# Optimization experiments

Hardware: AMD Instinct MI355X
Metric: run time of the kernel (lower is better)

The kernel has to match this reference:

```python
import jax, jax.numpy as jnp
import numpy as np

B, T, D = 4, 2048, 1024

def setup_inputs() -> dict:
    key = jax.random.key(0)
    kx, kq, kk, kv = jax.random.split(key, 4)
    return {
        "vector": jax.random.normal(kx, (B, T, D), dtype=jnp.float32),
        # original uses torch.rand -> uniform [0,1)
        "W_queries": jax.random.uniform(kq, (D, D), dtype=jnp.float32),
        "W_keys": jax.random.uniform(kk, (D, D), dtype=jnp.float32),
        "W_values": jax.random.uniform(kv, (D, D), dtype=jnp.float32),
    }

def reference(vector, W_queries, W_keys, W_values):
    b, num_token, d_out = vector.shape
    queries = vector @ W_queries          # [b, t, d]
    keys = vector @ W_keys                # [b, t, d]
    values = vector @ W_values            # [b, t, d]
    # attention_score: [b, q, k]
    scores = jnp.einsum('bqd,bkd->bqk', queries, keys)
    causal_mask = jnp.triu(jnp.ones((num_token, num_token), dtype=bool), k=1)
    scores = jnp.where(causal_mask[None, :, :], -jnp.inf, scores)
    # NOTE: original uses FLOOR division `//` by sqrt(d_k) -- faithful here.
    inv_sqrt_scale = jnp.asarray(np.sqrt(keys.shape[-1]), dtype=scores.dtype)
    weights = jnp.floor(scores / inv_sqrt_scale)
    # NOTE: original applies softmax over dim=1 (the query axis), not dim=-1.
    weights = jax.nn.softmax(weights, axis=1)
    # dropout rate is 0.0 (eval/deterministic): identity
    context = jnp.einsum('bqk,bkd->bqd', weights, values)
    return context
```

## Files before the change

### kernel.cpp

```cpp
#include <hip/hip_runtime.h>
#include <math.h>

typedef _Float16 half4 __attribute__((ext_vector_type(4)));
typedef _Float16 half8 __attribute__((ext_vector_type(8)));
typedef float f32x4 __attribute__((ext_vector_type(4)));

#define GLD16(gptr, lptr)                                                     \
    __builtin_amdgcn_global_load_lds(                                         \
        (const __attribute__((address_space(1))) unsigned int*)(gptr),        \
        (__attribute__((address_space(3))) unsigned int*)(lptr), 16, 0, 0)

#define WAIT_VM(N) asm volatile("s_waitcnt vmcnt(" #N ")" ::: "memory")
#define BARRIER()  __builtin_amdgcn_s_barrier()
#define SCHED_FENCE() __builtin_amdgcn_sched_barrier(0)

namespace {

constexpr int Bb = 4;
constexpr int Tt = 2048;
constexpr int Dd = 1024;
constexpr int BT = Bb * Tt;
constexpr int NCH = 16;

__device__ inline _Float16 f2h(float f) { return (_Float16)f; }

__global__ __launch_bounds__(256) void convert_all_kernel(
    const float* __restrict__ X,  const float* __restrict__ Wq,
    const float* __restrict__ Wk, const float* __restrict__ Wv,
    _Float16* __restrict__ Xhi, _Float16* __restrict__ Xlo,
    _Float16* __restrict__ Wqh, _Float16* __restrict__ Wql,
    _Float16* __restrict__ Wkh, _Float16* __restrict__ Wkl,
    _Float16* __restrict__ WvTh)
{
    __shared__ float tile[64][65];
    const int f = blockIdx.x;
    if (f < 8192) {
        const int idx = f * 1024 + threadIdx.x * 4;
        const float4 v = *(const float4*)(X + idx);
        const float a[4] = {v.x, v.y, v.z, v.w};
        half4 h, l;
#pragma unroll
        for (int i = 0; i < 4; ++i) {
            h[i] = f2h(a[i]);
            l[i] = f2h(a[i] - (float)h[i]);
        }
        *(half4*)(Xhi + idx) = h;
        *(half4*)(Xlo + idx) = l;
    } else if (f < 10240) {
        const int g = f - 8192;
        const int mat = g >> 10;
        const float* W = mat ? Wk : Wq;
        _Float16* Hh = mat ? Wkh : Wqh;
        _Float16* Ll = mat ? Wkl : Wql;
        const int idx = (g & 1023) * 1024 + threadIdx.x * 4;
        const float4 v = *(const float4*)(W + idx);
        const float a[4] = {v.x, v.y, v.z, v.w};
        half4 h, l;
#pragma unroll
        for (int i = 0; i < 4; ++i) {
            h[i] = f2h(a[i]);
            l[i] = f2h(a[i] - (float)h[i]);
        }
        *(half4*)(Hh + idx) = h;
        *(half4*)(Ll + idx) = l;
    } else {
        const int g = f - 10240;
        const int n0 = (g & 15) * 64, k0 = (g >> 4) * 64;
        const int tx = threadIdx.x & 63, ty = threadIdx.x >> 6;
#pragma unroll
        for (int i = 0; i < 16; ++i)
            tile[ty + i * 4][tx] = Wv[(size_t)(k0 + ty + i * 4) * Dd + n0 + tx];
        __syncthreads();
#pragma unroll
        for (int i = 0; i < 16; ++i) {
            const float v = tile[tx][ty + i * 4];
            WvTh[(size_t)(n0 + ty + i * 4) * Dd + k0 + tx] = f2h(v);
        }
    }
}

__global__ __launch_bounds__(256) void gt_kernel(
    const _Float16* __restrict__ Wkh, const _Float16* __restrict__ Wkl,
    const _Float16* __restrict__ Wqh, const _Float16* __restrict__ Wql,
    _Float16* __restrict__ GTh, _Float16* __restrict__ GTl)
{
    __shared__ _Float16 Ahl[2][2][4][512];
    __shared__ _Float16 Bhl[2][2][4][512];

    const int n0 = blockIdx.x * 64;
    const int m0 = blockIdx.y * 64;
    const int tid = threadIdx.x;
    const int w = tid >> 6, lane = tid & 63;
    const int lr = lane & 15, lq = lane >> 4;
    const int wi = (w >> 1) * 2, wj = (w & 1) * 2;

    f32x4 acc[2][2];
#pragma unroll
    for (int i = 0; i < 2; ++i)
#pragma unroll
        for (int j = 0; j < 2; ++j)
#pragma unroll
            for (int c = 0; c < 4; ++c) acc[i][j][c] = 0.f;

    auto stage = [&](int bf, int kk) {
        const int s = w;
        const size_t ar = (size_t)(m0 + s * 16 + lr) * Dd + kk + lq * 8;
        const size_t br = (size_t)(n0 + s * 16 + lr) * Dd + kk + lq * 8;
        GLD16(Wkh + ar, &Ahl[bf][0][s][0]);
        GLD16(Wkl + ar, &Ahl[bf][1][s][0]);
        GLD16(Wqh + br, &Bhl[bf][0][s][0]);
        GLD16(Wql + br, &Bhl[bf][1][s][0]);
    };

    stage(0, 0);
    int ib = 0;
    for (int step = 0; step < 32; ++step, ib ^= 1) {
        if (step < 31) {
            stage(ib ^ 1, (step + 1) << 5);
            WAIT_VM(4);
        } else {
            WAIT_VM(0);
        }
        BARRIER();
        SCHED_FENCE();
        half8 ah[2], al[2], bh[2], bl[2];
#pragma unroll
        for (int i = 0; i < 2; ++i) {
            ah[i] = *(const half8*)&Ahl[ib][0][wi + i][lane * 8];
            al[i] = *(const half8*)&Ahl[ib][1][wi + i][lane * 8];
        }
#pragma unroll
        for (int j = 0; j < 2; ++j) {
            bh[j] = *(const half8*)&Bhl[ib][0][wj + j][lane * 8];
            bl[j] = *(const half8*)&Bhl[ib][1][wj + j][lane * 8];
        }
#pragma unroll
        for (int i = 0; i < 2; ++i)
#pragma unroll
            for (int j = 0; j < 2; ++j) {
                acc[i][j] = __builtin_amdgcn_mfma_f32_16x16x32_f16(ah[i], bh[j], acc[i][j], 0, 0, 0);
                acc[i][j] = __builtin_amdgcn_mfma_f32_16x16x32_f16(ah[i], bl[j], acc[i][j], 0, 0, 0);
                acc[i][j] = __builtin_amdgcn_mfma_f32_16x16x32_f16(al[i], bh[j], acc[i][j], 0, 0, 0);
            }
        BARRIER();
    }

#pragma unroll
    for (int i = 0; i < 2; ++i)
#pragma unroll
        for (int r = 0; r < 4; ++r) {
            const int row = m0 + (wi + i) * 16 + lq * 4 + r;
#pragma unroll
            for (int j = 0; j < 2; ++j) {
                const int col = n0 + (wj + j) * 16 + lr;
                const float v = acc[i][j][r];
                const _Float16 h = f2h(v);
                GTh[(size_t)row * Dd + col] = h;
                GTl[(size_t)row * Dd + col] = f2h(v - (float)h);
            }
        }
}

__global__ __launch_bounds__(256, 2) void tv_kernel(
    const _Float16* __restrict__ Xhi, const _Float16* __restrict__ Xlo,
    const _Float16* __restrict__ GTh, const _Float16* __restrict__ GTl,
    const _Float16* __restrict__ WvTh,
    _Float16* __restrict__ Thi, _Float16* __restrict__ Tlo,
    _Float16* __restrict__ Vt)
{
    __shared__ _Float16 smem[32768];
    auto A_ = [&](int bf, int hl, int s) -> _Float16* {
        return smem + ((bf * 2 + hl) * 8 + s) * 512;
    };
    auto B_ = [&](int bf, int hl, int s) -> _Float16* {
        return smem + 16384 + ((bf * 2 + hl) * 8 + s) * 512;
    };

    const int f  = blockIdx.x;
    const int fp = (f & 7) * 128 + (f >> 3);
    const int mb  = fp >> 4;
    const int sub = fp & 15;
    const int m0 = mb * 128;
    const int n0 = (sub & 7) * 128;

    const int tid = threadIdx.x;
    const int w = tid >> 6, lane = tid & 63;
    const int lr = lane & 15, lq = lane >> 4;
    const int wr = (w >> 1) * 4, wc = (w & 1) * 4;

    f32x4 acc[4][4];
#pragma unroll
    for (int i = 0; i < 4; ++i)
#pragma unroll
        for (int j = 0; j < 4; ++j)
#pragma unroll
            for (int c = 0; c < 4; ++c) acc[i][j][c] = 0.f;

    if (sub < 8) {
        auto stage = [&](int bf, int kk) {
#pragma unroll
            for (int s2 = 0; s2 < 2; ++s2) {
                const int s = w * 2 + s2;
                const size_t ar = (size_t)(m0 + s * 16 + lr) * Dd + kk + lq * 8;
                const size_t br = (size_t)(n0 + s * 16 + lr) * Dd + kk + lq * 8;
                GLD16(Xhi + ar, A_(bf, 0, s));
                GLD16(Xlo + ar, A_(bf, 1, s));
                GLD16(GTh + br, B_(bf, 0, s));
                GLD16(GTl + br, B_(bf, 1, s));
            }
        };
        stage(0, 0);
        int ib = 0;
        for (int step = 0; step < 32; ++step, ib ^= 1) {
            if (step < 31) {
                stage(ib ^ 1, (step + 1) << 5);
                WAIT_VM(8);
            } else {
                WAIT_VM(0);
            }
            BARRIER();
            SCHED_FENCE();
            half8 ah[4], al[4], bh[4], bl[4];
#pragma unroll
            for (int i = 0; i < 4; ++i) {
                ah[i] = *(const half8*)(A_(ib, 0, wr + i) + lane * 8);
                al[i] = *(const half8*)(A_(ib, 1, wr + i) + lane * 8);
            }
#pragma unroll
            for (int j = 0; j < 4; ++j) {
                bh[j] = *(const half8*)(B_(ib, 0, wc + j) + lane * 8);
                bl[j] = *(const half8*)(B_(ib, 1, wc + j) + lane * 8);
            }
#pragma unroll
            for (int i = 0; i < 4; ++i)
#pragma unroll
                for (int j = 0; j < 4; ++j) {
                    acc[i][j] = __builtin_amdgcn_mfma_f32_16x16x32_f16(ah[i], bh[j], acc[i][j], 0, 0, 0);
                    acc[i][j] = __builtin_amdgcn_mfma_f32_16x16x32_f16(ah[i], bl[j], acc[i][j], 0, 0, 0);
                    acc[i][j] = __builtin_amdgcn_mfma_f32_16x16x32_f16(al[i], bh[j], acc[i][j], 0, 0, 0);
                }
            BARRIER();
        }
#pragma unroll
        for (int i = 0; i < 4; ++i)
#pragma unroll
            for (int r = 0; r < 4; ++r) {
                const int row = m0 + (wr + i) * 16 + lq * 4 + r;
#pragma unroll
                for (int j = 0; j < 4; ++j) {
                    const int col = n0 + (wc + j) * 16 + lr;
                    const float v = acc[i][j][r];
                    const _Float16 h = f2h(v);
                    Thi[(size_t)row * Dd + col] = h;
                    Tlo[(size_t)row * Dd + col] = f2h(v - (float)h);
                }
            }
    } else {
        auto stage = [&](int bf, int kk) {
#pragma unroll
            for (int s2 = 0; s2 < 2; ++s2) {
                const int s = w * 2 + s2;
                GLD16(Xhi + (size_t)(m0 + s * 16 + lr) * Dd + kk + lq * 8, A_(bf, 0, s));
                GLD16(WvTh + (size_t)(n0 + s * 16 + lr) * Dd + kk + lq * 8, B_(bf, 0, s));
            }
        };
        stage(0, 0);
        int ib = 0;
        for (int step = 0; step < 32; ++step, ib ^= 1) {
            if (step < 31) {
                stage(ib ^ 1, (step + 1) << 5);
                WAIT_VM(4);
            } else {
                WAIT_VM(0);
            }
            BARRIER();
            SCHED_FENCE();
            half8 a[4], b2[4];
#pragma unroll
            for (int i = 0; i < 4; ++i) a[i] = *(const half8*)(A_(ib, 0, wr + i) + lane * 8);
#pragma unroll
            for (int j = 0; j < 4; ++j) b2[j] = *(const half8*)(B_(ib, 0, wc + j) + lane * 8);
#pragma unroll
            for (int i = 0; i < 4; ++i)
#pragma unroll
                for (int j = 0; j < 4; ++j)
                    acc[i][j] = __builtin_amdgcn_mfma_f32_16x16x32_f16(a[i], b2[j], acc[i][j], 0, 0, 0);
            BARRIER();
        }
        __syncthreads();
#pragma unroll
        for (int i = 0; i < 4; ++i)
#pragma unroll
            for (int r2 = 0; r2 < 4; ++r2) {
                const int rloc = (wr + i) * 16 + lq * 4 + r2;
#pragma unroll
                for (int j = 0; j < 4; ++j) {
                    const int cloc = (wc + j) * 16 + lr;
                    smem[cloc * 136 + rloc] = f2h(acc[i][j][r2]);
                }
            }
        __syncthreads();
        const int b2i = m0 >> 11;
        const int t0  = m0 & 2047;
        const int dloc = tid >> 1, tl = (tid & 1) * 64;
        _Float16* vp = Vt + (size_t)b2i * Dd * Tt + (size_t)(n0 + dloc) * Tt + t0 + tl;
#pragma unroll
        for (int e = 0; e < 8; ++e)
            *(half8*)(vp + e * 8) = *(const half8*)&smem[dloc * 136 + tl + e * 8];
    }
}

__global__ __launch_bounds__(256, 2) void scores_mfma_kernel(
    const _Float16* __restrict__ Thi, const _Float16* __restrict__ Tlo,
    const _Float16* __restrict__ Xhi, const _Float16* __restrict__ Xlo,
    _Float16* __restrict__ Pp, float* __restrict__ Pm, float* __restrict__ Pl)
{
    const int f  = blockIdx.x;
    const int fp = (f & 7) * 68 + (f >> 3);
    const int b = fp / 136;
    const int t = fp - b * 136;
    int byi = (int)((sqrtf(8.f * t + 1.f) - 1.f) * 0.5f);
    if ((byi + 1) * (byi + 2) / 2 <= t) ++byi;
    if (byi * (byi + 1) / 2 > t) --byi;
    const int bxi = t - byi * (byi + 1) / 2;
    const int j0 = bxi * 128, q0 = byi * 128;
    _Float16* Pb = Pp + (size_t)b * Tt * Tt;

    __shared__ _Float16 Ahl[2][2][8][512];
    __shared__ _Float16 Bhl[2][2][8][512];
    const _Float16* Th = Thi + (size_t)b * Tt * Dd;
    const _Float16* Tl = Tlo + (size_t)b * Tt * Dd;
    const _Float16* Xh = Xhi + (size_t)b * Tt * Dd;
    const _Float16* Xl = Xlo + (size_t)b * Tt * Dd;

    const int tid = threadIdx.x;
    const int w = tid >> 6, lane = tid & 63;
    const int lr = lane & 15, lq = lane >> 4;
    const int wr = (w >> 1) * 4, wc = (w & 1) * 4;

    f32x4 acc[4][4];
#pragma unroll
    for (int i = 0; i < 4; ++i)
#pragma unroll
        for (int j = 0; j < 4; ++j)
#pragma unroll
            for (int c = 0; c < 4; ++c) acc[i][j][c] = 0.f;

    auto stage = [&](int bf, int kk) {
#pragma unroll
        for (int s2 = 0; s2 < 2; ++s2) {
            const int s = w * 2 + s2;
            const size_t ar = (size_t)(q0 + s * 16 + lr) * Dd + kk + lq * 8;
            const size_t br = (size_t)(j0 + s * 16 + lr) * Dd + kk + lq * 8;
            GLD16(Th + ar, &Ahl[bf][0][s][0]);
            GLD16(Tl + ar, &Ahl[bf][1][s][0]);
            GLD16(Xh + br, &Bhl[bf][0][s][0]);
            GLD16(Xl + br, &Bhl[bf][1][s][0]);
        }
    };

    stage(0, 0);
    int ib = 0;
    for (int step = 0; step < 32; ++step, ib ^= 1) {
        if (step < 31) {
            stage(ib ^ 1, (step + 1) << 5);
            WAIT_VM(8);
        } else {
            WAIT_VM(0);
        }
        BARRIER();
        SCHED_FENCE();
        half8 ah[4], al[4], bh[4], bl[4];
#pragma unroll
        for (int i = 0; i < 4; ++i) {
            ah[i] = *(const half8*)&Ahl[ib][0][wr + i][lane * 8];
            al[i] = *(const half8*)&Ahl[ib][1][wr + i][lane * 8];
        }
#pragma unroll
        for (int j = 0; j < 4; ++j) {
            bh[j] = *(const half8*)&Bhl[ib][0][wc + j][lane * 8];
            bl[j] = *(const half8*)&Bhl[ib][1][wc + j][lane * 8];
        }
#pragma unroll
        for (int i = 0; i < 4; ++i)
#pragma unroll
            for (int j = 0; j < 4; ++j) {
                acc[i][j] = __builtin_amdgcn_mfma_f32_16x16x32_f16(ah[i], bh[j], acc[i][j], 0, 0, 0);
                acc[i][j] = __builtin_amdgcn_mfma_f32_16x16x32_f16(ah[i], bl[j], acc[i][j], 0, 0, 0);
                acc[i][j] = __builtin_amdgcn_mfma_f32_16x16x32_f16(al[i], bh[j], acc[i][j], 0, 0, 0);
            }
        BARRIER();
    }

    float sv[4][4][4];
#pragma unroll
    for (int i = 0; i < 4; ++i)
#pragma unroll
        for (int r = 0; r < 4; ++r) {
            const int q = q0 + (wr + i) * 16 + lq * 4 + r;
#pragma unroll
            for (int j = 0; j < 4; ++j) {
                const int jg = j0 + (wc + j) * 16 + lr;
                sv[i][j][r] = (jg <= q) ? floorf(acc[i][j][r] * 0.03125f) : -INFINITY;
            }
        }

    float* red  = (float*)&Ahl[0][0][0][0];
    float* colm = red + 2048;
    __syncthreads();
    for (int e = tid; e < 2048; e += 256) red[e] = -INFINITY;
    __syncthreads();
    const int rowidx = (w * 4 + lq) * 128;
#pragma unroll
    for (int j = 0; j < 4; ++j) {
        const int c = (wc + j) * 16 + lr;
        float lm = -INFINITY;
#pragma unroll
        for (int i = 0; i < 4; ++i)
#pragma unroll
            for (int r = 0; r < 4; ++r) lm = fmaxf(lm, sv[i][j][r]);
        red[rowidx + c] = lm;
    }
    __syncthreads();
    if (tid < 128) {
        float m = -INFINITY;
#pragma unroll
        for (int e = 0; e < 16; ++e) m = fmaxf(m, red[e * 128 + tid]);
        colm[tid] = m;
    }
    __syncthreads();
    float ls[4];
#pragma unroll
    for (int j = 0; j < 4; ++j) {
        const int c = (wc + j) * 16 + lr;
        const int jg = j0 + c;
        const float m = colm[c];
        float s = 0.f;
#pragma unroll
        for (int i = 0; i < 4; ++i)
#pragma unroll
            for (int r = 0; r < 4; ++r) {
                const float e = __expf(sv[i][j][r] - m);
                s += e;
                const int q = q0 + (wr + i) * 16 + lq * 4 + r;
                Pb[(size_t)q * Tt + jg] = f2h(e);
            }
        ls[j] = s;
    }
    __syncthreads();
    for (int e = tid; e < 2048; e += 256) red[e] = 0.f;
    __syncthreads();
#pragma unroll
    for (int j = 0; j < 4; ++j) red[rowidx + (wc + j) * 16 + lr] = ls[j];
    __syncthreads();
    if (tid < 128) {
        float l = 0.f;
#pragma unroll
        for (int e = 0; e < 16; ++e) l += red[e * 128 + tid];
        const size_t o = ((size_t)b * NCH + byi) * Tt + j0 + tid;
        Pm[o] = colm[tid];
        Pl[o] = l;
    }
}

__global__ __launch_bounds__(256) void colstats_merge_kernel(
    const float* __restrict__ Pm, const float* __restrict__ Pl,
    float* __restrict__ Mb, float* __restrict__ Lb)
{
    const int j = blockIdx.x * 256 + threadIdx.x;
    const int b = blockIdx.y;
    const int jt = j >> 7;
    float m = -INFINITY, l = 0.f;
    for (int c = jt; c < NCH; ++c) {
        const size_t pidx = ((size_t)b * NCH + c) * Tt + j;
        const float mi = Pm[pidx];
        if (mi == -INFINITY) continue;
        const float li = Pl[pidx];
        if (mi > m) { l = l * __expf(m - mi) + li; m = mi; }
        else        { l += li * __expf(mi - m); }
    }
    Mb[(size_t)b * Tt + j] = m;
    Lb[(size_t)b * Tt + j] = (l > 0.f) ? 1.f / l : 0.f;
}

__global__ __launch_bounds__(256) void context_mfma_kernel(
    const _Float16* __restrict__ Pp, const float* __restrict__ Pm,
    const float* __restrict__ Mb, const float* __restrict__ Lb,
    const _Float16* __restrict__ Vt, float* __restrict__ Out)
{
    __shared__ _Float16 As[8][512];
    __shared__ _Float16 Bl[2][8][512];
    __shared__ float cbuf[2048];

    const int f  = blockIdx.x;
    const int fp = (f & 7) * 64 + (f >> 3);
    const int b  = fp >> 7;
    const int r  = fp & 127;
    const int bx = r & 7;
    const int tq = r >> 3;
    const int by = (tq & 1) ? (15 - (tq >> 1)) : (tq >> 1);
    const int d0 = bx * 128;
    const int q0 = by * 128;
    const _Float16* Pb = Pp + (size_t)b * Tt * Tt;
    const float* Pmb = Pm + ((size_t)b * NCH + by) * Tt;
    const float* Mp = Mb + (size_t)b * Tt;
    const float* Lp = Lb + (size_t)b * Tt;
    const _Float16* Vb = Vt + (size_t)b * Dd * Tt;
    float* Ob = Out + (size_t)b * Tt * Dd;

    const int tid = threadIdx.x;
    const int w = tid >> 6, lane = tid & 63;
    const int lr = lane & 15, lq = lane >> 4;
    const int wr = (w >> 1) * 4, wc = (w & 1) * 4;
    const int kmax = q0 + 128;

    for (int k = tid; k < kmax; k += 256)
        cbuf[k] = __expf(Pmb[k] - Mp[k]) * Lp[k];

    f32x4 acc[4][4];
#pragma unroll
    for (int i = 0; i < 4; ++i)
#pragma unroll
        for (int j = 0; j < 4; ++j)
#pragma unroll
            for (int c = 0; c < 4; ++c) acc[i][j][c] = 0.f;

    half8 areg[2];
    auto loadA = [&](int k0) {
#pragma unroll
        for (int s2 = 0; s2 < 2; ++s2) {
            const int s = w * 2 + s2;
            areg[s2] = *(const half8*)(Pb + (size_t)(q0 + s * 16 + lr) * Tt + k0 + lq * 8);
        }
    };
    auto issueV = [&](int ib2, int k0) {
#pragma unroll
        for (int s2 = 0; s2 < 2; ++s2) {
            const int s = w * 2 + s2;
            GLD16(Vb + (size_t)(d0 + s * 16 + lr) * Tt + k0 + lq * 8, &Bl[ib2][s][0]);
        }
    };
    auto writeA = [&](int k0) {
        const float* cp = cbuf + k0 + lq * 8;
        float cv[8];
#pragma unroll
        for (int e = 0; e < 8; ++e) cv[e] = cp[e];
#pragma unroll
        for (int s2 = 0; s2 < 2; ++s2) {
            const int s = w * 2 + s2;
            half8 out;
#pragma unroll
            for (int e = 0; e < 8; ++e) out[e] = f2h((float)areg[s2][e] * cv[e]);
            *(half8*)&As[s][lane * 8] = out;
        }
    };

    __syncthreads();
    loadA(0);
    issueV(0, 0);
    writeA(0);
    __syncthreads();

    int ib = 0;
    const int nstep = kmax >> 5;
    for (int step = 0; step < nstep; ++step, ib ^= 1) {
        const bool more = (step + 1 < nstep);
        if (more) {
            loadA((step + 1) << 5);
            issueV(ib ^ 1, (step + 1) << 5);
        }
        half8 a[4], b2[4];
#pragma unroll
        for (int i = 0; i < 4; ++i) a[i] = *(const half8*)&As[wr + i][lane * 8];
#pragma unroll
        for (int j = 0; j < 4; ++j) b2[j] = *(const half8*)&Bl[ib][wc + j][lane * 8];
#pragma unroll
        for (int i = 0; i < 4; ++i)
#pragma unroll
            for (int j = 0; j < 4; ++j)
                acc[i][j] = __builtin_amdgcn_mfma_f32_16x16x32_f16(a[i], b2[j], acc[i][j], 0, 0, 0);
        BARRIER();
        SCHED_FENCE();
        if (more) {
            writeA((step + 1) << 5);
            __syncthreads();
        }
    }

#pragma unroll
    for (int i = 0; i < 4; ++i)
#pragma unroll
        for (int r2 = 0; r2 < 4; ++r2) {
            const int row = q0 + (wr + i) * 16 + lq * 4 + r2;
#pragma unroll
            for (int j = 0; j < 4; ++j)
                Ob[(size_t)row * Dd + d0 + (wc + j) * 16 + lr] = acc[i][j][r2];
        }
}

}

extern "C" void kernel_launch(void* const* d_in, const int* in_sizes, int n_in,
                              void* d_out, int out_size, void* d_ws, size_t ws_size,
                              hipStream_t stream)
{
    const float* X  = (const float*)d_in[0];
    const float* Wq = (const float*)d_in[1];
    const float* Wk = (const float*)d_in[2];
    const float* Wv = (const float*)d_in[3];

    char* ws = (char*)d_ws;
    const size_t MB = 1024 * 1024;
    _Float16* Xhi  = (_Float16*)ws;
    _Float16* Xlo  = (_Float16*)(ws + 16 * MB);
    _Float16* Wqh  = (_Float16*)(ws + 32 * MB);
    _Float16* Wql  = (_Float16*)(ws + 34 * MB);
    _Float16* Wkh  = (_Float16*)(ws + 36 * MB);
    _Float16* Wkl  = (_Float16*)(ws + 38 * MB);
    _Float16* WvTh = (_Float16*)(ws + 40 * MB);
    _Float16* GTh  = (_Float16*)(ws + 44 * MB);
    _Float16* GTl  = (_Float16*)(ws + 46 * MB);
    _Float16* Thi  = (_Float16*)(ws + 48 * MB);
    _Float16* Tlo  = (_Float16*)(ws + 64 * MB);
    _Float16* Vt   = (_Float16*)(ws + 80 * MB);
    _Float16* Pp   = (_Float16*)(ws + 112 * MB);
    float*    Mb   = (float*)(ws + 176 * MB);
    float*    Lb   = Mb + (size_t)Bb * Tt;
    float*    Pm   = Lb + (size_t)Bb * Tt;
    float*    Pl   = Pm + (size_t)Bb * NCH * Tt;
    float*    Out  = (float*)d_out;

    convert_all_kernel<<<10496, 256, 0, stream>>>(X, Wq, Wk, Wv, Xhi, Xlo,
                                                  Wqh, Wql, Wkh, Wkl, WvTh);
    gt_kernel<<<dim3(16, 16), 256, 0, stream>>>(Wkh, Wkl, Wqh, Wql, GTh, GTl);
    tv_kernel<<<dim3(1024), 256, 0, stream>>>(Xhi, Xlo, GTh, GTl, WvTh, Thi, Tlo, Vt);
    scores_mfma_kernel<<<dim3(544), 256, 0, stream>>>(Thi, Tlo, Xhi, Xlo, Pp, Pm, Pl);
    colstats_merge_kernel<<<dim3(Tt / 256, Bb), 256, 0, stream>>>(Pm, Pl, Mb, Lb);
    context_mfma_kernel<<<dim3(512), 256, 0, stream>>>(Pp, Pm, Mb, Lb, Vt, Out);
}
```

Measured before the change: 440.9 us.

## Double-buffer A tile and prefetch P two steps ahead with explicit waitcnts

The context kernel's scaled-P tile in LDS becomes double-buffered. The loop is unrolled by two, so P loads for step i+2 and i+3 are issued in registers ahead of time. The old per-step pair of barriers is replaced by one barrier per step, with manual vmcnt/lgkmcnt waits so writeA overlaps with MFMA work. This raises register and LDS use and relies on hand-counted vmcnt values being correct. nstep is always even here, so the unrolled loop is valid.

```diff
diff --git a/kernel.cpp b/kernel.cpp
--- a/kernel.cpp
+++ b/kernel.cpp
@@ -11,6 +11,7 @@
         (__attribute__((address_space(3))) unsigned int*)(lptr), 16, 0, 0)
 
 #define WAIT_VM(N) asm volatile("s_waitcnt vmcnt(" #N ")" ::: "memory")
+#define WAIT_LGKM0() asm volatile("s_waitcnt lgkmcnt(0)" ::: "memory")
 #define BARRIER()  __builtin_amdgcn_s_barrier()
 #define SCHED_FENCE() __builtin_amdgcn_sched_barrier(0)
 
@@ -488,7 +489,7 @@
     const float* __restrict__ Mb, const float* __restrict__ Lb,
     const _Float16* __restrict__ Vt, float* __restrict__ Out)
 {
-    __shared__ _Float16 As[8][512];
+    __shared__ _Float16 As[2][8][512];
     __shared__ _Float16 Bl[2][8][512];
     __shared__ float cbuf[2048];
 
@@ -513,6 +514,7 @@
     const int lr = lane & 15, lq = lane >> 4;
     const int wr = (w >> 1) * 4, wc = (w & 1) * 4;
     const int kmax = q0 + 128;
+    const int nstep = kmax >> 5;
 
     for (int k = tid; k < kmax; k += 256)
         cbuf[k] = __expf(Pmb[k] - Mp[k]) * Lp[k];
@@ -525,22 +527,22 @@
 #pragma unroll
             for (int c = 0; c < 4; ++c) acc[i][j][c] = 0.f;
 
-    half8 areg[2];
-    auto loadA = [&](int k0) {
+    half8 RpA[2], RpB[2];
+    auto loadP = [&](half8 (&R)[2], int k0) {
 #pragma unroll
         for (int s2 = 0; s2 < 2; ++s2) {
             const int s = w * 2 + s2;
-            areg[s2] = *(const half8*)(Pb + (size_t)(q0 + s * 16 + lr) * Tt + k0 + lq * 8);
-        }
-    };
-    auto issueV = [&](int ib2, int k0) {
+            R[s2] = *(const half8*)(Pb + (size_t)(q0 + s * 16 + lr) * Tt + k0 + lq * 8);
+        }
+    };
+    auto issueV = [&](int bf, int k0) {
 #pragma unroll
         for (int s2 = 0; s2 < 2; ++s2) {
             const int s = w * 2 + s2;
-            GLD16(Vb + (size_t)(d0 + s * 16 + lr) * Tt + k0 + lq * 8, &Bl[ib2][s][0]);
-        }
-    };
-    auto writeA = [&](int k0) {
+            GLD16(Vb + (size_t)(d0 + s * 16 + lr) * Tt + k0 + lq * 8, &Bl[bf][s][0]);
+        }
+    };
+    auto writeA = [&](int bf, half8 (&R)[2], int k0) {
         const float* cp = cbuf + k0 + lq * 8;
         float cv[8];
 #pragma unroll
@@ -550,40 +552,58 @@
             const int s = w * 2 + s2;
             half8 out;
 #pragma unroll
-            for (int e = 0; e < 8; ++e) out[e] = f2h((float)areg[s2][e] * cv[e]);
-            *(half8*)&As[s][lane * 8] = out;
-        }
-    };
-
-    __syncthreads();
-    loadA(0);
-    issueV(0, 0);
-    writeA(0);
-    __syncthreads();
-
-    int ib = 0;
-    const int nstep = kmax >> 5;
-    for (int step = 0; step < nstep; ++step, ib ^= 1) {
-        const bool more = (step + 1 < nstep);
-        if (more) {
-            loadA((step + 1) << 5);
-            issueV(ib ^ 1, (step + 1) << 5);
-        }
+            for (int e = 0; e < 8; ++e) out[e] = f2h((float)R[s2][e] * cv[e]);
+            *(half8*)&As[bf][s][lane * 8] = out;
+        }
+    };
+    auto domfma = [&](int bf) {
         half8 a[4], b2[4];
 #pragma unroll
-        for (int i = 0; i < 4; ++i) a[i] = *(const half8*)&As[wr + i][lane * 8];
-#pragma unroll
-        for (int j = 0; j < 4; ++j) b2[j] = *(const half8*)&Bl[ib][wc + j][lane * 8];
+        for (int i = 0; i < 4; ++i) a[i] = *(const half8*)&As[bf][wr + i][lane * 8];
+#pragma unroll
+        for (int j = 0; j < 4; ++j) b2[j] = *(const half8*)&Bl[bf][wc + j][lane * 8];
 #pragma unroll
         for (int i = 0; i < 4; ++i)
 #pragma unroll
             for (int j = 0; j < 4; ++j)
                 acc[i][j] = __builtin_amdgcn_mfma_f32_16x16x32_f16(a[i], b2[j], acc[i][j], 0, 0, 0);
-        BARRIER();
-        SCHED_FENCE();
-        if (more) {
-            writeA((step + 1) << 5);
-            __syncthreads();
+    };
+
+    __syncthreads();
+
+    issueV(0, 0);
+    loadP(RpA, 0);
+    loadP(RpB, 32);
+    WAIT_VM(2);
+    writeA(0, RpA, 0);
+    WAIT_LGKM0();
+    BARRIER();
+
+    for (int i = 0; i < nstep; i += 2) {
+        {
+            const bool pfP = (i + 2 < nstep);
+            issueV(1, (i + 1) << 5);
+            if (pfP) loadP(RpA, (i + 2) << 5);
+            domfma(0);
+            if (pfP) WAIT_VM(4); else WAIT_VM(2);
+            writeA(1, RpB, (i + 1) << 5);
+            if (pfP) WAIT_VM(2); else WAIT_VM(0);
+            WAIT_LGKM0();
+            BARRIER();
+        }
+        {
+            const bool pfV = (i + 2 < nstep);
+            const bool pfP = (i + 3 < nstep);
+            if (pfV) issueV(0, (i + 2) << 5);
+            if (pfP) loadP(RpB, (i + 3) << 5);
+            domfma(1);
+            if (pfV) {
+                if (pfP) WAIT_VM(4); else WAIT_VM(2);
+                writeA(0, RpA, (i + 2) << 5);
+                if (pfP) WAIT_VM(2); else WAIT_VM(0);
+                WAIT_LGKM0();
+            }
+            BARRIER();
         }
     }
 
```

Measured after the change: 421.0 us. 4.5% less time.
